# Kernel optimization log

Hardware: AMD Instinct MI355X
Metric: run time of the kernel (lower is better)

The kernel has to match this reference:

```python
import jax, jax.numpy as jnp
import numpy as np

B, T, DIM, H, BUCKET = 4, 4096, 1024, 16, 64
E = DIM // H          # head dim = 64
U = T // BUCKET       # number of buckets = 64
EPS = 1e-6


def setup_inputs() -> dict:
    key = jax.random.key(0)
    ks = jax.random.split(key, 5)
    scale = 1.0 / np.sqrt(DIM)
    return {
        "x": jax.random.normal(ks[0], (B, T, DIM), dtype=jnp.float32),
        "Wq": jax.random.normal(ks[1], (DIM, DIM), dtype=jnp.float32) * scale,
        "Wk": jax.random.normal(ks[2], (DIM, DIM), dtype=jnp.float32) * scale,
        "Wv": jax.random.normal(ks[3], (DIM, DIM), dtype=jnp.float32) * scale,
        "Wo": jax.random.normal(ks[4], (DIM, DIM), dtype=jnp.float32) * scale,
        "bo": jnp.zeros((DIM,), dtype=jnp.float32),
    }


def _causal_linear_attn(q, k, v):
    # q, k, v: [b, h, t, e]; psi(k) = elu(k) + 1; q softmaxed over feature dim
    q = jax.nn.softmax(q, axis=-1)
    k = jax.nn.elu(k) + 1.0
    bucket = lambda x: x.reshape(*x.shape[:-2], U, BUCKET, E)  # [b,h,u,n,e]
    b_q, b_k, b_v = bucket(q), bucket(k), bucket(v)
    # cumulative key sums per bucket: [b,h,u,d]
    b_k_cumsum = jnp.cumsum(b_k.sum(axis=-2), axis=2)
    # per-bucket context then cumulative over buckets: [b,h,u,d,e]
    context = jnp.einsum("bhund,bhune->bhude", b_k, b_v)
    context = jnp.cumsum(context, axis=2)
    context = context / (b_k_cumsum[..., None] + EPS)
    # shift by one bucket (blindspot): bucket u sees context through bucket u-1
    context = jnp.concatenate(
        [jnp.zeros_like(context[:, :, :1]), context[:, :, :-1]], axis=2
    )
    attn = jnp.einsum("bhund,bhude->bhune", b_q, context)
    return attn.reshape(q.shape)  # [b,h,t,e]


def reference(x, Wq, Wk, Wv, Wo, bo):
    b, t, _ = x.shape
    q = x @ Wq
    k = x @ Wk
    v = x @ Wv
    merge = lambda z: z.reshape(b, t, H, E).transpose(0, 2, 1, 3)  # [b,h,t,e]
    attn = _causal_linear_attn(merge(q), merge(k), merge(v))
    out = attn.transpose(0, 2, 1, 3).reshape(b, t, DIM)
    return out @ Wo + bo
```

## Files before the change

kernel.cpp:

```cpp
#include <hip/hip_runtime.h>


#define T_LEN 4096
#define DIMN  1024
#define NHEAD 16
#define NB    4
#define MROWS (NB * T_LEN)

typedef float f32x4 __attribute__((ext_vector_type(4)));
typedef short s16x8 __attribute__((ext_vector_type(8)));
typedef short s16x4 __attribute__((ext_vector_type(4)));
using u16 = unsigned short;

__device__ __forceinline__ u16 f2bf(float f) {
  unsigned int u = __float_as_uint(f);
  u += 0x7fffu + ((u >> 16) & 1u);
  return (u16)(u >> 16);
}
__device__ __forceinline__ float bf2f(u16 h) {
  return __uint_as_float(((unsigned int)h) << 16);
}
__device__ __forceinline__ int swz16k(int off) {
  return off ^ (((off >> 7) & 3) << 4);
}

__global__ __launch_bounds__(256) void cvt_w_kern(const float* __restrict__ W,
                                                  u16* __restrict__ WT) {
  __shared__ float tile[64][65];
  const int blk = blockIdx.x;
  const int k0 = (blk >> 4) << 6;
  const int n0 = (blk & 15) << 6;
  const int tid = threadIdx.x;
  const int r = tid >> 6;
  const int c = tid & 63;
#pragma unroll
  for (int i = 0; i < 16; ++i) {
    int row = (i << 2) + r;
    tile[row][c] = W[(size_t)(k0 + row) * DIMN + n0 + c];
  }
  __syncthreads();
#pragma unroll
  for (int i = 0; i < 16; ++i) {
    int row = (i << 2) + r;
    WT[(size_t)(n0 + row) * DIMN + k0 + c] = f2bf(tile[c][row]);
  }
}

__global__ __launch_bounds__(256) void cvt_x_kern(const float* __restrict__ x,
                                                  u16* __restrict__ xb) {
  size_t i = ((size_t)blockIdx.x * 256 + threadIdx.x) * 4;
  f32x4 v = *(const f32x4*)(x + i);
  s16x4 o;
  o.x = (short)f2bf(v.x); o.y = (short)f2bf(v.y);
  o.z = (short)f2bf(v.z); o.w = (short)f2bf(v.w);
  *(s16x4*)(xb + i) = o;
}

template <int MODE>
__global__ __launch_bounds__(512, 2) void gemm256(
    const u16* __restrict__ A, const u16* __restrict__ Bt,
    u16* __restrict__ dq, u16* __restrict__ dk, u16* __restrict__ dv,
    float* __restrict__ dO, const float* __restrict__ bias) {
  constexpr int K = 1024;
  constexpr int BNT = (MODE == 0) ? 12 : 4;
  constexpr int NT = K / 64;
  extern __shared__ char lds[];

  const int tid = threadIdx.x;
  const int l = tid & 63;
  const int w = tid >> 6;
  const int wm = w >> 2;
  const int wn = w & 3;

  const int nwg = (int)gridDim.x;
  const int bid = (int)blockIdx.x;
  const int swz = (bid & 7) * (nwg >> 3) + (bid >> 3);
  const int bm = swz / BNT, bn = swz % BNT;
  const size_t arow0 = (size_t)bm * 256;
  const size_t brow0 = (size_t)bn * 256;

  int lrow[2], lcol[2];
#pragma unroll
  for (int i = 0; i < 2; ++i) {
    int lg = swz16k(tid * 16 + i * 8192);
    lrow[i] = lg >> 6;
    lcol[i] = (lg & 63) >> 1;
  }

  const int fr = l & 15;
  const int kswz = (((l >> 4) << 4)) ^ ((((fr >> 1) & 3)) << 4);

  auto STAGE = [&](int matsel, int kh, int tt) {
    const int kbase = (tt & (NT - 1)) * 64 + kh * 32;
#pragma unroll
    for (int i = 0; i < 2; ++i) {
      const u16* src = (matsel == 0)
          ? A  + (arow0 + (size_t)lrow[i]) * K + kbase + lcol[i]
          : Bt + (brow0 + (size_t)lrow[i]) * K + kbase + lcol[i];
      char* dst = lds + ((tt & 1) * 65536 + (matsel * 2 + kh) * 16384 +
                         i * 8192 + w * 1024);
      __builtin_amdgcn_global_load_lds(
          (__attribute__((address_space(1))) const void*)src,
          (__attribute__((address_space(3))) void*)dst, 16, 0, 0);
    }
  };
  auto LDA = [&](int buf, int kh, int rowb) -> s16x8 {
    return *(const s16x8*)(lds + buf * 65536 + kh * 16384 + rowb * 64 + kswz);
  };
  auto LDB = [&](int buf, int kh, int rowb) -> s16x8 {
    return *(const s16x8*)(lds + buf * 65536 + 32768 + kh * 16384 + rowb * 64 + kswz);
  };

  f32x4 acc[8][4];
#pragma unroll
  for (int i = 0; i < 8; ++i)
#pragma unroll
    for (int j = 0; j < 4; ++j) acc[i][j] = {0.f, 0.f, 0.f, 0.f};

  STAGE(0, 0, 0); STAGE(1, 0, 0); STAGE(0, 1, 0); STAGE(1, 1, 0);
  STAGE(0, 0, 1); STAGE(1, 0, 1);
  asm volatile("s_waitcnt vmcnt(8)" ::: "memory");
  __builtin_amdgcn_sched_barrier(0);
  __builtin_amdgcn_s_barrier();

  const int amb = wm * 128;
  const int bnb = wn * 64;
  s16x8 af[4], bfr[4];

  for (int t = 0; t < NT; ++t) {
    const int buf = t & 1;
#pragma unroll
    for (int i = 0; i < 4; ++i) af[i]  = LDA(buf, 0, amb + i * 16 + fr);
#pragma unroll
    for (int i = 0; i < 4; ++i) bfr[i] = LDB(buf, 0, bnb + i * 16 + fr);
    STAGE(0, 1, t + 1);
    __builtin_amdgcn_s_barrier();
    asm volatile("s_waitcnt lgkmcnt(0)" ::: "memory");
    __builtin_amdgcn_sched_barrier(0);
    __builtin_amdgcn_s_setprio(1);
#pragma unroll
    for (int mi = 0; mi < 4; ++mi)
#pragma unroll
      for (int ni = 0; ni < 4; ++ni)
        acc[mi][ni] = __builtin_amdgcn_mfma_f32_16x16x32_bf16(
            af[mi], bfr[ni], acc[mi][ni], 0, 0, 0);
    __builtin_amdgcn_s_setprio(0);
    __builtin_amdgcn_s_barrier();
#pragma unroll
    for (int i = 0; i < 4; ++i) af[i] = LDA(buf, 0, amb + (4 + i) * 16 + fr);
    STAGE(1, 1, t + 1);
    __builtin_amdgcn_s_barrier();
    asm volatile("s_waitcnt lgkmcnt(0)" ::: "memory");
    __builtin_amdgcn_sched_barrier(0);
    __builtin_amdgcn_s_setprio(1);
#pragma unroll
    for (int mi = 0; mi < 4; ++mi)
#pragma unroll
      for (int ni = 0; ni < 4; ++ni)
        acc[4 + mi][ni] = __builtin_amdgcn_mfma_f32_16x16x32_bf16(
            af[mi], bfr[ni], acc[4 + mi][ni], 0, 0, 0);
    __builtin_amdgcn_s_setprio(0);
    asm volatile("s_waitcnt vmcnt(8)" ::: "memory");
    __builtin_amdgcn_sched_barrier(0);
    __builtin_amdgcn_s_barrier();
#pragma unroll
    for (int i = 0; i < 4; ++i) af[i]  = LDA(buf, 1, amb + i * 16 + fr);
#pragma unroll
    for (int i = 0; i < 4; ++i) bfr[i] = LDB(buf, 1, bnb + i * 16 + fr);
    STAGE(0, 0, t + 2);
    __builtin_amdgcn_s_barrier();
    asm volatile("s_waitcnt lgkmcnt(0)" ::: "memory");
    __builtin_amdgcn_sched_barrier(0);
    __builtin_amdgcn_s_setprio(1);
#pragma unroll
    for (int mi = 0; mi < 4; ++mi)
#pragma unroll
      for (int ni = 0; ni < 4; ++ni)
        acc[mi][ni] = __builtin_amdgcn_mfma_f32_16x16x32_bf16(
            af[mi], bfr[ni], acc[mi][ni], 0, 0, 0);
    __builtin_amdgcn_s_setprio(0);
    __builtin_amdgcn_s_barrier();
#pragma unroll
    for (int i = 0; i < 4; ++i) af[i] = LDA(buf, 1, amb + (4 + i) * 16 + fr);
    STAGE(1, 0, t + 2);
    __builtin_amdgcn_s_barrier();
    asm volatile("s_waitcnt lgkmcnt(0)" ::: "memory");
    __builtin_amdgcn_sched_barrier(0);
    __builtin_amdgcn_s_setprio(1);
#pragma unroll
    for (int mi = 0; mi < 4; ++mi)
#pragma unroll
      for (int ni = 0; ni < 4; ++ni)
        acc[4 + mi][ni] = __builtin_amdgcn_mfma_f32_16x16x32_bf16(
            af[mi], bfr[ni], acc[4 + mi][ni], 0, 0, 0);
    __builtin_amdgcn_s_setprio(0);
    asm volatile("s_waitcnt vmcnt(8)" ::: "memory");
    __builtin_amdgcn_sched_barrier(0);
    __builtin_amdgcn_s_barrier();
  }

  const int r0 = (l >> 4) << 2;
  const int c0 = l & 15;
  if constexpr (MODE == 0) {
    const int mat = bn >> 2;
    u16* dst = (mat == 0) ? dq : ((mat == 1) ? dk : dv);
    const size_t colbase = (size_t)(bn & 3) * 256 + (size_t)wn * 64;
    if (mat == 0) {
#pragma unroll
      for (int mi = 0; mi < 8; ++mi) {
#pragma unroll
        for (int j = 0; j < 4; ++j) {
          float v0 = acc[mi][0][j], v1 = acc[mi][1][j];
          float v2 = acc[mi][2][j], v3 = acc[mi][3][j];
          float m = fmaxf(fmaxf(v0, v1), fmaxf(v2, v3));
#pragma unroll
          for (int off = 1; off < 16; off <<= 1) m = fmaxf(m, __shfl_xor(m, off));
          float e0 = __expf(v0 - m), e1 = __expf(v1 - m);
          float e2 = __expf(v2 - m), e3 = __expf(v3 - m);
          float s = e0 + e1 + e2 + e3;
#pragma unroll
          for (int off = 1; off < 16; off <<= 1) s += __shfl_xor(s, off);
          float inv = 1.f / s;
          const size_t row = arow0 + wm * 128 + mi * 16 + r0 + j;
          u16* p = dst + row * DIMN + colbase + c0;
          p[0]  = f2bf(e0 * inv); p[16] = f2bf(e1 * inv);
          p[32] = f2bf(e2 * inv); p[48] = f2bf(e3 * inv);
        }
      }
    } else {
#pragma unroll
      for (int mi = 0; mi < 8; ++mi)
#pragma unroll
        for (int ni = 0; ni < 4; ++ni)
#pragma unroll
          for (int j = 0; j < 4; ++j) {
            const size_t row = arow0 + wm * 128 + mi * 16 + r0 + j;
            float v = acc[mi][ni][j];
            float r = (mat == 1) ? (v > 0.f ? v + 1.f : __expf(v)) : v;
            dst[row * DIMN + colbase + ni * 16 + c0] = f2bf(r);
          }
    }
  } else {
    const size_t colbase = brow0 + (size_t)wn * 64;
#pragma unroll
    for (int mi = 0; mi < 8; ++mi)
#pragma unroll
      for (int ni = 0; ni < 4; ++ni) {
        const size_t col = colbase + ni * 16 + c0;
        const float bv = bias[col];
#pragma unroll
        for (int j = 0; j < 4; ++j) {
          const size_t row = arow0 + wm * 128 + mi * 16 + r0 + j;
          dO[row * DIMN + col] = acc[mi][ni][j] + bv;
        }
      }
  }
}

__global__ __launch_bounds__(256) void ctx_bucket_kern(const u16* __restrict__ kb,
                                                       const u16* __restrict__ vb,
                                                       float* __restrict__ ctx,
                                                       float* __restrict__ ksum) {
  __shared__ float kl[4096];
  __shared__ float vl[4096];
  const int blk = blockIdx.x;
  const int u = blk & 63;
  const int bh = blk >> 6;
  const int b = bh >> 4, h = bh & 15;
  const size_t rowbase = (size_t)b * T_LEN + (size_t)u * 64;
  const int tid = threadIdx.x;
#pragma unroll
  for (int i = 0; i < 16; ++i) {
    int idx = i * 256 + tid;
    int n = idx >> 6, d = idx & 63;
    size_t g = (rowbase + n) * DIMN + (size_t)h * 64 + d;
    kl[idx] = bf2f(kb[g]);
    vl[idx] = bf2f(vb[g]);
  }
  __syncthreads();
  const int dq = (tid & 15) << 2;
  const int eq = (tid >> 4) << 2;
  float a[4][4] = {};
  float ks[4] = {};
  for (int n = 0; n < 64; ++n) {
    f32x4 kv = *(const f32x4*)&kl[n * 64 + dq];
    f32x4 vv = *(const f32x4*)&vl[n * 64 + eq];
#pragma unroll
    for (int i = 0; i < 4; ++i) {
      ks[i] += kv[i];
#pragma unroll
      for (int j = 0; j < 4; ++j) a[i][j] += kv[i] * vv[j];
    }
  }
  const size_t cbase = (size_t)blk * 4096;
#pragma unroll
  for (int i = 0; i < 4; ++i) {
    f32x4 o = {a[i][0], a[i][1], a[i][2], a[i][3]};
    *(f32x4*)&ctx[cbase + (size_t)(dq + i) * 64 + eq] = o;
  }
  if ((tid >> 4) == 0) {
    f32x4 o = {ks[0], ks[1], ks[2], ks[3]};
    *(f32x4*)&ksum[(size_t)blk * 64 + dq] = o;
  }
}

__global__ __launch_bounds__(256) void ctx_cumnorm_kern(float* __restrict__ ctx,
                                                        const float* __restrict__ ksum) {
  const int tid = blockIdx.x * 256 + threadIdx.x;
  const int bh = tid >> 12;
  const int rem = tid & 4095;
  const int d = rem >> 6;
  const int e = rem & 63;
  float c = 0.f, accK = 0.f;
  for (int u = 0; u < 64; ++u) {
    const size_t base = ((size_t)(bh * 64 + u)) * 4096 + (size_t)d * 64 + e;
    float cv = ctx[base];
    float kk = ksum[(size_t)(bh * 64 + u) * 64 + d];
    float o = (u == 0) ? 0.f : c / (accK + 1e-6f);
    ctx[base] = o;
    c += cv; accK += kk;
  }
}

__global__ __launch_bounds__(256) void attn_bucket_kern(const u16* __restrict__ qb,
                                                        const float* __restrict__ ctx,
                                                        u16* __restrict__ attn) {
  __shared__ float qT[64 * 68];
  __shared__ float cl[4096];
  const int blk = blockIdx.x;
  const int u = blk & 63;
  const int bh = blk >> 6;
  const int b = bh >> 4, h = bh & 15;
  const size_t rowbase = (size_t)b * T_LEN + (size_t)u * 64;
  const int tid = threadIdx.x;
  const size_t cbase = (size_t)blk * 4096;
#pragma unroll
  for (int i = 0; i < 16; ++i) {
    int idx = i * 256 + tid;
    int n = idx >> 6, d = idx & 63;
    qT[d * 68 + n] = bf2f(qb[(rowbase + n) * DIMN + (size_t)h * 64 + d]);
    cl[idx] = ctx[cbase + idx];
  }
  __syncthreads();
  const int nq = (tid & 15) << 2;
  const int eq = (tid >> 4) << 2;
  float a[4][4] = {};
  for (int d = 0; d < 64; ++d) {
    f32x4 qv = *(const f32x4*)&qT[d * 68 + nq];
    f32x4 cv = *(const f32x4*)&cl[d * 64 + eq];
#pragma unroll
    for (int i = 0; i < 4; ++i)
#pragma unroll
      for (int j = 0; j < 4; ++j) a[i][j] += qv[i] * cv[j];
  }
#pragma unroll
  for (int i = 0; i < 4; ++i) {
    s16x4 o;
    o.x = (short)f2bf(a[i][0]); o.y = (short)f2bf(a[i][1]);
    o.z = (short)f2bf(a[i][2]); o.w = (short)f2bf(a[i][3]);
    *(s16x4*)&attn[(rowbase + nq + i) * DIMN + (size_t)h * 64 + eq] = o;
  }
}

extern "C" void kernel_launch(void* const* d_in, const int* in_sizes, int n_in,
                              void* d_out, int out_size, void* d_ws, size_t ws_size,
                              hipStream_t stream) {
  const float* x  = (const float*)d_in[0];
  const float* Wq = (const float*)d_in[1];
  const float* Wk = (const float*)d_in[2];
  const float* Wv = (const float*)d_in[3];
  const float* Wo = (const float*)d_in[4];
  const float* bo = (const float*)d_in[5];
  float* out = (float*)d_out;

  constexpr size_t SZ_XB = (size_t)MROWS * DIMN * 2;
  constexpr size_t SZ_WT = (size_t)DIMN * DIMN * 2;
  constexpr size_t SZ_CTX = (size_t)NB * NHEAD * 64 * 64 * 64 * 4;
  char* ws = (char*)d_ws;
  u16*   xb   = (u16*)(ws);
  u16*   wqT  = (u16*)(ws + SZ_XB);
  u16*   wkT  = (u16*)(ws + SZ_XB + SZ_WT);
  u16*   wvT  = (u16*)(ws + SZ_XB + 2 * SZ_WT);
  u16*   woT  = (u16*)(ws + SZ_XB + 3 * SZ_WT);
  u16*   qb   = (u16*)(ws + SZ_XB + 4 * SZ_WT);
  u16*   kb   = (u16*)(ws + 2 * SZ_XB + 4 * SZ_WT);
  u16*   vb   = (u16*)(ws + 3 * SZ_XB + 4 * SZ_WT);
  float* ctx  = (float*)(ws + 4 * SZ_XB + 4 * SZ_WT);
  float* ksum = (float*)(ws + 4 * SZ_XB + 4 * SZ_WT + SZ_CTX);
  u16*   attn = xb;

  (void)hipFuncSetAttribute((const void*)gemm256<0>,
                            hipFuncAttributeMaxDynamicSharedMemorySize, 131072);
  (void)hipFuncSetAttribute((const void*)gemm256<1>,
                            hipFuncAttributeMaxDynamicSharedMemorySize, 131072);

  cvt_w_kern<<<256, 256, 0, stream>>>(Wq, wqT);
  cvt_w_kern<<<256, 256, 0, stream>>>(Wk, wkT);
  cvt_w_kern<<<256, 256, 0, stream>>>(Wv, wvT);
  cvt_w_kern<<<256, 256, 0, stream>>>(Wo, woT);
  cvt_x_kern<<<MROWS * DIMN / 4 / 256, 256, 0, stream>>>(x, xb);

  gemm256<0><<<768, 512, 131072, stream>>>(xb, wqT, qb, kb, vb, nullptr, nullptr);

  ctx_bucket_kern<<<NB * NHEAD * 64, 256, 0, stream>>>(kb, vb, ctx, ksum);
  ctx_cumnorm_kern<<<1024, 256, 0, stream>>>(ctx, ksum);
  attn_bucket_kern<<<NB * NHEAD * 64, 256, 0, stream>>>(qb, ctx, attn);

  gemm256<1><<<256, 512, 131072, stream>>>(attn, woT, nullptr, nullptr, nullptr, out, bo);
}
```

Baseline: 287.1 us.

## Stage GEMM epilogues through LDS, trim main-loop barriers, merge weight conversions

Both GEMM epilogues now write results into a swizzled LDS tile and then emit wide, row-contiguous global stores. This replaces the scattered 2-byte and 4-byte per-lane stores of the QKV and output projections. In the main loop, the extra s_barrier and lgkmcnt(0) waits between the fragment loads and the MFMA blocks are removed, leaving the compiler to insert the register-dependency waits. The four weight-transpose launches are merged into a single 1024-block launch. Risks are LDS reuse hazards at the epilogue boundary, now guarded by a full vmcnt wait and barrier, and possible races from the relaxed in-loop synchronisation.

New measurement: 284.4 us. About the same (-1.0%).

```diff
diff --git a/kernel.cpp b/kernel.cpp
--- a/kernel.cpp
+++ b/kernel.cpp
@@ -24,10 +24,16 @@
   return off ^ (((off >> 7) & 3) << 4);
 }
 
-__global__ __launch_bounds__(256) void cvt_w_kern(const float* __restrict__ W,
+__global__ __launch_bounds__(256) void cvt_w_kern(const float* __restrict__ W0,
+                                                  const float* __restrict__ W1,
+                                                  const float* __restrict__ W2,
+                                                  const float* __restrict__ W3,
                                                   u16* __restrict__ WT) {
   __shared__ float tile[64][65];
-  const int blk = blockIdx.x;
+  const int blk = blockIdx.x & 255;
+  const int sel = blockIdx.x >> 8;
+  const float* W = (sel == 0) ? W0 : (sel == 1) ? W1 : (sel == 2) ? W2 : W3;
+  u16* dst = WT + (size_t)sel * DIMN * DIMN;
   const int k0 = (blk >> 4) << 6;
   const int n0 = (blk & 15) << 6;
   const int tid = threadIdx.x;
@@ -42,7 +48,7 @@
 #pragma unroll
   for (int i = 0; i < 16; ++i) {
     int row = (i << 2) + r;
-    WT[(size_t)(n0 + row) * DIMN + k0 + c] = f2bf(tile[c][row]);
+    dst[(size_t)(n0 + row) * DIMN + k0 + c] = f2bf(tile[c][row]);
   }
 }
 
@@ -129,14 +135,12 @@
 
   for (int t = 0; t < NT; ++t) {
     const int buf = t & 1;
+    __builtin_amdgcn_sched_barrier(0);
 #pragma unroll
     for (int i = 0; i < 4; ++i) af[i]  = LDA(buf, 0, amb + i * 16 + fr);
 #pragma unroll
     for (int i = 0; i < 4; ++i) bfr[i] = LDB(buf, 0, bnb + i * 16 + fr);
     STAGE(0, 1, t + 1);
-    __builtin_amdgcn_s_barrier();
-    asm volatile("s_waitcnt lgkmcnt(0)" ::: "memory");
-    __builtin_amdgcn_sched_barrier(0);
     __builtin_amdgcn_s_setprio(1);
 #pragma unroll
     for (int mi = 0; mi < 4; ++mi)
@@ -146,12 +150,10 @@
             af[mi], bfr[ni], acc[mi][ni], 0, 0, 0);
     __builtin_amdgcn_s_setprio(0);
     __builtin_amdgcn_s_barrier();
+    __builtin_amdgcn_sched_barrier(0);
 #pragma unroll
     for (int i = 0; i < 4; ++i) af[i] = LDA(buf, 0, amb + (4 + i) * 16 + fr);
     STAGE(1, 1, t + 1);
-    __builtin_amdgcn_s_barrier();
-    asm volatile("s_waitcnt lgkmcnt(0)" ::: "memory");
-    __builtin_amdgcn_sched_barrier(0);
     __builtin_amdgcn_s_setprio(1);
 #pragma unroll
     for (int mi = 0; mi < 4; ++mi)
@@ -163,14 +165,12 @@
     asm volatile("s_waitcnt vmcnt(8)" ::: "memory");
     __builtin_amdgcn_sched_barrier(0);
     __builtin_amdgcn_s_barrier();
+    __builtin_amdgcn_sched_barrier(0);
 #pragma unroll
     for (int i = 0; i < 4; ++i) af[i]  = LDA(buf, 1, amb + i * 16 + fr);
 #pragma unroll
     for (int i = 0; i < 4; ++i) bfr[i] = LDB(buf, 1, bnb + i * 16 + fr);
     STAGE(0, 0, t + 2);
-    __builtin_amdgcn_s_barrier();
-    asm volatile("s_waitcnt lgkmcnt(0)" ::: "memory");
-    __builtin_amdgcn_sched_barrier(0);
     __builtin_amdgcn_s_setprio(1);
 #pragma unroll
     for (int mi = 0; mi < 4; ++mi)
@@ -180,12 +180,10 @@
             af[mi], bfr[ni], acc[mi][ni], 0, 0, 0);
     __builtin_amdgcn_s_setprio(0);
     __builtin_amdgcn_s_barrier();
+    __builtin_amdgcn_sched_barrier(0);
 #pragma unroll
     for (int i = 0; i < 4; ++i) af[i] = LDA(buf, 1, amb + (4 + i) * 16 + fr);
     STAGE(1, 0, t + 2);
-    __builtin_amdgcn_s_barrier();
-    asm volatile("s_waitcnt lgkmcnt(0)" ::: "memory");
-    __builtin_amdgcn_sched_barrier(0);
     __builtin_amdgcn_s_setprio(1);
 #pragma unroll
     for (int mi = 0; mi < 4; ++mi)
@@ -199,12 +197,16 @@
     __builtin_amdgcn_s_barrier();
   }
 
+  asm volatile("s_waitcnt vmcnt(0)" ::: "memory");
+  __builtin_amdgcn_sched_barrier(0);
+  __builtin_amdgcn_s_barrier();
+
   const int r0 = (l >> 4) << 2;
   const int c0 = l & 15;
   if constexpr (MODE == 0) {
+    u16* lt = (u16*)lds;
     const int mat = bn >> 2;
     u16* dst = (mat == 0) ? dq : ((mat == 1) ? dk : dv);
-    const size_t colbase = (size_t)(bn & 3) * 256 + (size_t)wn * 64;
     if (mat == 0) {
 #pragma unroll
       for (int mi = 0; mi < 8; ++mi) {
@@ -221,10 +223,13 @@
 #pragma unroll
           for (int off = 1; off < 16; off <<= 1) s += __shfl_xor(s, off);
           float inv = 1.f / s;
-          const size_t row = arow0 + wm * 128 + mi * 16 + r0 + j;
-          u16* p = dst + row * DIMN + colbase + c0;
-          p[0]  = f2bf(e0 * inv); p[16] = f2bf(e1 * inv);
-          p[32] = f2bf(e2 * inv); p[48] = f2bf(e3 * inv);
+          const int row = wm * 128 + mi * 16 + r0 + j;
+          const int sxr = ((row >> 2) & 7) << 4;
+          const int cb = wn * 64 + c0;
+          lt[row * 256 + ((cb) ^ sxr)]      = f2bf(e0 * inv);
+          lt[row * 256 + ((cb + 16) ^ sxr)] = f2bf(e1 * inv);
+          lt[row * 256 + ((cb + 32) ^ sxr)] = f2bf(e2 * inv);
+          lt[row * 256 + ((cb + 48) ^ sxr)] = f2bf(e3 * inv);
         }
       }
     } else {
@@ -234,26 +239,55 @@
         for (int ni = 0; ni < 4; ++ni)
 #pragma unroll
           for (int j = 0; j < 4; ++j) {
-            const size_t row = arow0 + wm * 128 + mi * 16 + r0 + j;
+            const int row = wm * 128 + mi * 16 + r0 + j;
+            const int col = wn * 64 + ni * 16 + c0;
             float v = acc[mi][ni][j];
             float r = (mat == 1) ? (v > 0.f ? v + 1.f : __expf(v)) : v;
-            dst[row * DIMN + colbase + ni * 16 + c0] = f2bf(r);
+            lt[row * 256 + (col ^ (((row >> 2) & 7) << 4))] = f2bf(r);
           }
     }
+    __builtin_amdgcn_s_barrier();
+    const size_t gcb = (size_t)(bn & 3) * 256;
+#pragma unroll
+    for (int i = 0; i < 16; ++i) {
+      const int cid = tid + i * 512;
+      const int r = cid >> 5;
+      const int g = (cid & 31) * 8;
+      const int pc = g ^ (((r >> 2) & 7) << 4);
+      s16x8 vv = *(const s16x8*)&lt[r * 256 + pc];
+      *(s16x8*)&dst[(arow0 + r) * DIMN + gcb + g] = vv;
+    }
   } else {
-    const size_t colbase = brow0 + (size_t)wn * 64;
-#pragma unroll
-    for (int mi = 0; mi < 8; ++mi)
-#pragma unroll
-      for (int ni = 0; ni < 4; ++ni) {
-        const size_t col = colbase + ni * 16 + c0;
-        const float bv = bias[col];
-#pragma unroll
-        for (int j = 0; j < 4; ++j) {
-          const size_t row = arow0 + wm * 128 + mi * 16 + r0 + j;
-          dO[row * DIMN + col] = acc[mi][ni][j] + bv;
-        }
+    float* lf = (float*)lds;
+#pragma unroll
+    for (int half = 0; half < 2; ++half) {
+      if (wm == half) {
+#pragma unroll
+        for (int mi = 0; mi < 8; ++mi)
+#pragma unroll
+          for (int ni = 0; ni < 4; ++ni) {
+            const int col = wn * 64 + ni * 16 + c0;
+            const float bv = bias[brow0 + col];
+#pragma unroll
+            for (int j = 0; j < 4; ++j) {
+              const int row = mi * 16 + r0 + j;
+              lf[row * 256 + (col ^ (((row >> 2) & 1) << 4))] =
+                  acc[mi][ni][j] + bv;
+            }
+          }
       }
+      __builtin_amdgcn_s_barrier();
+#pragma unroll
+      for (int i = 0; i < 16; ++i) {
+        const int cid = tid + i * 512;
+        const int r = cid >> 6;
+        const int g = (cid & 63) * 4;
+        const int pc = g ^ (((r >> 2) & 1) << 4);
+        f32x4 vv = *(const f32x4*)&lf[r * 256 + pc];
+        *(f32x4*)&dO[(arow0 + half * 128 + r) * DIMN + brow0 + g] = vv;
+      }
+      __builtin_amdgcn_s_barrier();
+    }
   }
 }
 
@@ -379,8 +413,6 @@
   char* ws = (char*)d_ws;
   u16*   xb   = (u16*)(ws);
   u16*   wqT  = (u16*)(ws + SZ_XB);
-  u16*   wkT  = (u16*)(ws + SZ_XB + SZ_WT);
-  u16*   wvT  = (u16*)(ws + SZ_XB + 2 * SZ_WT);
   u16*   woT  = (u16*)(ws + SZ_XB + 3 * SZ_WT);
   u16*   qb   = (u16*)(ws + SZ_XB + 4 * SZ_WT);
   u16*   kb   = (u16*)(ws + 2 * SZ_XB + 4 * SZ_WT);
@@ -394,10 +426,7 @@
   (void)hipFuncSetAttribute((const void*)gemm256<1>,
                             hipFuncAttributeMaxDynamicSharedMemorySize, 131072);
 
-  cvt_w_kern<<<256, 256, 0, stream>>>(Wq, wqT);
-  cvt_w_kern<<<256, 256, 0, stream>>>(Wk, wkT);
-  cvt_w_kern<<<256, 256, 0, stream>>>(Wv, wvT);
-  cvt_w_kern<<<256, 256, 0, stream>>>(Wo, woT);
+  cvt_w_kern<<<1024, 256, 0, stream>>>(Wq, Wk, Wv, Wo, wqT);
   cvt_x_kern<<<MROWS * DIMN / 4 / 256, 256, 0, stream>>>(x, xb);
 
   gemm256<0><<<768, 512, 131072, stream>>>(xb, wqT, qb, kb, vb, nullptr, nullptr);
```
